# Kernel optimization log

Measured on AMD Instinct MI355X. Metric: run time of the kernel, lower is better.

## Reference

```python
import jax, jax.numpy as jnp
import numpy as np

N_STEPS = 7
N_TERMS = 4


def _sobel_kernel2d():
    dx = jnp.array([[-1.0, 0.0, 1.0], [-2.0, 0.0, 2.0], [-1.0, 0.0, 1.0]], dtype=jnp.float32)
    dy = jnp.array([[-1.0, -2.0, -1.0], [0.0, 0.0, 0.0], [1.0, 2.0, 1.0]], dtype=jnp.float32)
    return 0.125 * jnp.stack([dy, dx, dy, dx], 0)[:, None]  # [4,1,3,3]


def _grid_sample_bilinear(src, sx, sy):
    # src: [N,C,H,W]; sx,sy: [N,H,W] pixel coords (align_corners=False, zeros padding)
    N, C, H, W = src.shape
    x0 = jnp.floor(sx)
    y0 = jnp.floor(sy)
    wx = (sx - x0)[:, None]  # [N,1,H,W]
    wy = (sy - y0)[:, None]
    x0i = x0.astype(jnp.int32)
    y0i = y0.astype(jnp.int32)

    def gather(yi, xi):
        valid = ((xi >= 0) & (xi < W) & (yi >= 0) & (yi < H))
        xc = jnp.clip(xi, 0, W - 1)
        yc = jnp.clip(yi, 0, H - 1)
        v = jax.vmap(lambda im, y, x: im[:, y, x])(src, yc, xc)  # [N,C,H,W]
        return v * valid[:, None].astype(src.dtype)

    v00 = gather(y0i, x0i)
    v01 = gather(y0i, x0i + 1)
    v10 = gather(y0i + 1, x0i)
    v11 = gather(y0i + 1, x0i + 1)
    return (v00 * (1 - wx) * (1 - wy) + v01 * wx * (1 - wy)
            + v10 * (1 - wx) * wy + v11 * wx * wy)


def _transform(src, disp, gy, gx, H, W):
    # new pixel locations; torch normalizes with (size-1) but samples with
    # align_corners=False, net mapping: p -> p*S/(S-1) - 0.5
    py = gy + disp[:, 0]
    px = gx + disp[:, 1]
    sy = py * (H / (H - 1)) - 0.5
    sx = px * (W / (W - 1)) - 0.5
    return _grid_sample_bilinear(src, sx, sy)


def _jacobian2d(vel):
    # replicate-pad then depthwise sobel conv -> [N,2,2,H,W]
    N, _, H, W = vel.shape
    padded = jnp.pad(vel, ((0, 0), (0, 0), (1, 1), (1, 1)), mode='edge')
    jac = jax.lax.conv_general_dilated(
        padded, _sobel_kernel2d(), window_strides=(1, 1), padding='VALID',
        feature_group_count=2, dimension_numbers=('NCHW', 'OIHW', 'NCHW'))
    return jac.reshape(N, 2, 2, H, W)


def _logdet1p(jac, eps):
    # -sum_n (-eps)^n tr(J^n)/n over the 2x2 dims, per pixel -> [N,H,W]
    ld = jnp.zeros(jac.shape[:1] + jac.shape[-2:], dtype=jac.dtype)
    xn = jac
    for n in range(1, N_TERMS + 1):
        if n > 1:
            xn = jnp.einsum('nikhw,nkjhw->nijhw', xn, jac)
        tr = xn[:, 0, 0] + xn[:, 1, 1]
        ld = ld - ((-eps) ** n) * tr / n
    return ld


def _integrate(vel, logdet_jac):
    N, _, H, W = vel.shape
    gy, gx = jnp.meshgrid(jnp.arange(H, dtype=vel.dtype),
                          jnp.arange(W, dtype=vel.dtype), indexing='ij')
    eps = 2.0 ** (-N_STEPS)
    disp = eps * vel
    if logdet_jac:
        ldjac = _logdet1p(_jacobian2d(vel), eps)[:, None]  # [N,1,H,W]
    else:
        ldjac = None
    for _ in range(N_STEPS):
        disp = disp + _transform(disp, disp, gy, gx, H, W)
        if logdet_jac:
            ldjac = ldjac + _transform(ldjac, disp, gy, gx, H, W)
    return disp, ldjac


def setup_inputs() -> dict:
    key = jax.random.key(0)
    vel = jax.random.normal(key, (16, 2, 512, 512), dtype=jnp.float32)
    return {"vel": vel, "logdet_jac": 1}


def reference(vel, logdet_jac):
    return _integrate(vel, bool(logdet_jac))
```

## Files before the change

### kernel.cpp

```cpp
#include <hip/hip_runtime.h>


#define NB 16
#define HH 512
#define WW 512
#define HW (HH * WW)
#define TOT (NB * HW)
#define EPS 0.0078125f
#define DISP_ELEMS (NB * 2 * HW)

typedef _Float16 f16;
typedef _Float16 f16x2 __attribute__((ext_vector_type(2)));

struct Samp {
    int i00, i01, i10, i11;
    float w00, w01, w10, w11;
};

__device__ __forceinline__ Samp make_samp(float sy, float sx) {
    float fy = floorf(sy), fx = floorf(sx);
    float wy = sy - fy, wx = sx - fx;
    int y0 = (int)fy, x0 = (int)fx;
    int y1 = y0 + 1, x1 = x0 + 1;
    bool xv0 = (unsigned)x0 < (unsigned)WW;
    bool xv1 = (unsigned)x1 < (unsigned)WW;
    bool yv0 = (unsigned)y0 < (unsigned)HH;
    bool yv1 = (unsigned)y1 < (unsigned)HH;
    int xc0 = min(max(x0, 0), WW - 1), xc1 = min(max(x1, 0), WW - 1);
    int yc0 = min(max(y0, 0), HH - 1), yc1 = min(max(y1, 0), HH - 1);
    Samp s;
    s.i00 = yc0 * WW + xc0; s.i01 = yc0 * WW + xc1;
    s.i10 = yc1 * WW + xc0; s.i11 = yc1 * WW + xc1;
    float omwx = 1.0f - wx, omwy = 1.0f - wy;
    s.w00 = (xv0 && yv0) ? omwx * omwy : 0.0f;
    s.w01 = (xv1 && yv0) ? wx * omwy   : 0.0f;
    s.w10 = (xv0 && yv1) ? omwx * wy   : 0.0f;
    s.w11 = (xv1 && yv1) ? wx * wy     : 0.0f;
    return s;
}

__global__ void __launch_bounds__(256) init_kernel(const float* __restrict__ vel,
                                                   f16x2* __restrict__ ddst,
                                                   f16* __restrict__ ldst) {
    int idx = blockIdx.x * 256 + threadIdx.x;
    int n = idx >> 18;
    int rem = idx & (HW - 1);
    int y = rem >> 9, x = rem & (WW - 1);

    const float* v0 = vel + (size_t)n * 2 * HW;
    const float* v1 = v0 + HW;

    float c0 = v0[rem], c1 = v1[rem];
    f16x2 dd; dd.x = (f16)(EPS * c0); dd.y = (f16)(EPS * c1);
    ddst[(size_t)n * HW + rem] = dd;

    int ym = max(y - 1, 0), yp = min(y + 1, HH - 1);
    int xm = max(x - 1, 0), xp = min(x + 1, WW - 1);
    int rmm = ym * WW + xm, rm0 = ym * WW + x, rmp = ym * WW + xp;
    int r0m = y * WW + xm,                    r0p = y * WW + xp;
    int rpm = yp * WW + xm, rp0 = yp * WW + x, rpp = yp * WW + xp;

    float a, b, c, d;
    {
        float tmm = v0[rmm], tm0 = v0[rm0], tmp = v0[rmp];
        float t0m = v0[r0m],                t0p = v0[r0p];
        float tpm = v0[rpm], tp0 = v0[rp0], tpp = v0[rpp];
        a = 0.125f * ((tpm + 2.0f * tp0 + tpp) - (tmm + 2.0f * tm0 + tmp));
        b = 0.125f * ((tmp + 2.0f * t0p + tpp) - (tmm + 2.0f * t0m + tpm));
    }
    {
        float tmm = v1[rmm], tm0 = v1[rm0], tmp = v1[rmp];
        float t0m = v1[r0m],                t0p = v1[r0p];
        float tpm = v1[rpm], tp0 = v1[rp0], tpp = v1[rpp];
        c = 0.125f * ((tpm + 2.0f * tp0 + tpp) - (tmm + 2.0f * tm0 + tmp));
        d = 0.125f * ((tmp + 2.0f * t0p + tpp) - (tmm + 2.0f * t0m + tpm));
    }

    float xa = a, xb = b, xc = c, xd = d;
    float ld = EPS * (xa + xd);
    float na = xa * a + xb * c, nb = xa * b + xb * d;
    float nc = xc * a + xd * c, nd = xc * b + xd * d;
    xa = na; xb = nb; xc = nc; xd = nd;
    ld -= (EPS * EPS) * (xa + xd) * 0.5f;
    na = xa * a + xb * c; nb = xa * b + xb * d;
    nc = xc * a + xd * c; nd = xc * b + xd * d;
    xa = na; xb = nb; xc = nc; xd = nd;
    ld += (EPS * EPS * EPS) * (xa + xd) * (1.0f / 3.0f);
    na = xa * a + xb * c;
    nd = xc * b + xd * d;
    ld -= (EPS * EPS * EPS * EPS) * (na + nd) * 0.25f;

    ldst[(size_t)n * HW + rem] = (f16)ld;
}

template <bool FINAL>
__global__ void __launch_bounds__(256) step_kernel(const f16x2* __restrict__ dsrc,
                                                   const f16* __restrict__ lsrc,
                                                   f16x2* __restrict__ ddst,
                                                   f16* __restrict__ ldst,
                                                   float* __restrict__ doutp,
                                                   float* __restrict__ loutp) {
    int bid = blockIdx.x;
    int task = ((bid & 7) << 11) | (bid >> 3);
    int idx = task * 256 + threadIdx.x;
    int n = idx >> 18;
    int rem = idx & (HW - 1);
    int y = rem >> 9, x = rem & (WW - 1);

    const float SC = 512.0f / 511.0f;

    const f16x2* dp = dsrc + (size_t)n * HW;
    f16x2 dv = dp[rem];
    float d0 = (float)dv.x, d1 = (float)dv.y;

    float sy = ((float)y + d0) * SC - 0.5f;
    float sx = ((float)x + d1) * SC - 0.5f;
    Samp s = make_samp(sy, sx);

    f16x2 g00 = dp[s.i00], g01 = dp[s.i01], g10 = dp[s.i10], g11 = dp[s.i11];
    float nd0 = d0 + s.w00 * (float)g00.x + s.w01 * (float)g01.x
                   + s.w10 * (float)g10.x + s.w11 * (float)g11.x;
    float nd1 = d1 + s.w00 * (float)g00.y + s.w01 * (float)g01.y
                   + s.w10 * (float)g10.y + s.w11 * (float)g11.y;

    if (FINAL) {
        float* pd = doutp + (size_t)n * 2 * HW;
        pd[rem] = nd0;
        pd[HW + rem] = nd1;
    } else {
        f16x2 w; w.x = (f16)nd0; w.y = (f16)nd1;
        ddst[(size_t)n * HW + rem] = w;
    }

    float sy2 = ((float)y + nd0) * SC - 0.5f;
    float sx2 = ((float)x + nd1) * SC - 0.5f;
    Samp s2 = make_samp(sy2, sx2);

    const f16* lp = lsrc + (size_t)n * HW;
    float l = (float)lp[rem];
    float nl = l + s2.w00 * (float)lp[s2.i00] + s2.w01 * (float)lp[s2.i01]
                 + s2.w10 * (float)lp[s2.i10] + s2.w11 * (float)lp[s2.i11];
    if (FINAL) {
        loutp[(size_t)n * HW + rem] = nl;
    } else {
        ldst[(size_t)n * HW + rem] = (f16)nl;
    }
}

extern "C" void kernel_launch(void* const* d_in, const int* in_sizes, int n_in,
                              void* d_out, int out_size, void* d_ws, size_t ws_size,
                              hipStream_t stream) {
    const float* vel = (const float*)d_in[0];
    float* out = (float*)d_out;

    f16*   baseA = (f16*)d_out;
    f16*   baseB = (f16*)d_ws;
    f16x2* dA = (f16x2*)baseA;
    f16*   lA = baseA + (size_t)2 * TOT;
    f16x2* dB = (f16x2*)baseB;
    f16*   lB = baseB + (size_t)2 * TOT;

    dim3 grid(TOT / 256), block(256);

    init_kernel<<<grid, block, 0, stream>>>(vel, dB, lB);

    const f16x2* ds = dB;
    const f16*   ls = lB;
    for (int s = 0; s < 6; ++s) {
        f16x2* dd  = (s & 1) ? dB : dA;
        f16*   ldd = (s & 1) ? lB : lA;
        step_kernel<false><<<grid, block, 0, stream>>>(ds, ls, dd, ldd, nullptr, nullptr);
        ds = dd; ls = ldd;
    }
    step_kernel<true><<<grid, block, 0, stream>>>(ds, ls, nullptr, nullptr,
                                                  out, out + DISP_ELEMS);
}
```

Measured before the change: 143.9 us.

## Skew ldjac update one step so both fields share the same bilinear samples

In the reference, each step's ldjac update samples at the freshly updated displacement. That position is the same one the next step's displacement update samples at. The pipeline is restructured into a displacement-only first step, then fused steps that sample disp(k) and ldjac(k-1) with a single set of indices and weights, then a final step that only updates ldjac and writes out. This removes the second make_samp and the dependent second gather round per step, and lets the displacement and ldjac gathers issue together. The cost is an extra kernel launch, and all buffers now live in the workspace, which needs about 48 MB.

```diff
diff --git a/kernel.cpp b/kernel.cpp
--- a/kernel.cpp
+++ b/kernel.cpp
@@ -8,6 +8,7 @@
 #define TOT (NB * HW)
 #define EPS 0.0078125f
 #define DISP_ELEMS (NB * 2 * HW)
+#define SC (512.0f / 511.0f)
 
 typedef _Float16 f16;
 typedef _Float16 f16x2 __attribute__((ext_vector_type(2)));
@@ -93,28 +94,25 @@
     ldst[(size_t)n * HW + rem] = (f16)ld;
 }
 
-template <bool FINAL>
-__global__ void __launch_bounds__(256) step_kernel(const f16x2* __restrict__ dsrc,
-                                                   const f16* __restrict__ lsrc,
-                                                   f16x2* __restrict__ ddst,
-                                                   f16* __restrict__ ldst,
-                                                   float* __restrict__ doutp,
-                                                   float* __restrict__ loutp) {
+__device__ __forceinline__ int remap_idx() {
     int bid = blockIdx.x;
     int task = ((bid & 7) << 11) | (bid >> 3);
-    int idx = task * 256 + threadIdx.x;
-    int n = idx >> 18;
-    int rem = idx & (HW - 1);
-    int y = rem >> 9, x = rem & (WW - 1);
-
-    const float SC = 512.0f / 511.0f;
+    return task * 256 + threadIdx.x;
+}
+
+__global__ void __launch_bounds__(256) step_disp(const f16x2* __restrict__ dsrc,
+                                                 f16x2* __restrict__ ddst) {
+    int idx = remap_idx();
+    int n = idx >> 18;
+    int rem = idx & (HW - 1);
+    int y = rem >> 9, x = rem & (WW - 1);
 
     const f16x2* dp = dsrc + (size_t)n * HW;
     f16x2 dv = dp[rem];
     float d0 = (float)dv.x, d1 = (float)dv.y;
 
-    float sy = ((float)y + d0) * SC - 0.5f;
-    float sx = ((float)x + d1) * SC - 0.5f;
+    float sy = fmaf((float)y + d0, SC, -0.5f);
+    float sx = fmaf((float)x + d1, SC, -0.5f);
     Samp s = make_samp(sy, sx);
 
     f16x2 g00 = dp[s.i00], g01 = dp[s.i01], g10 = dp[s.i10], g11 = dp[s.i11];
@@ -123,28 +121,72 @@
     float nd1 = d1 + s.w00 * (float)g00.y + s.w01 * (float)g01.y
                    + s.w10 * (float)g10.y + s.w11 * (float)g11.y;
 
-    if (FINAL) {
-        float* pd = doutp + (size_t)n * 2 * HW;
-        pd[rem] = nd0;
-        pd[HW + rem] = nd1;
-    } else {
-        f16x2 w; w.x = (f16)nd0; w.y = (f16)nd1;
-        ddst[(size_t)n * HW + rem] = w;
-    }
-
-    float sy2 = ((float)y + nd0) * SC - 0.5f;
-    float sx2 = ((float)x + nd1) * SC - 0.5f;
-    Samp s2 = make_samp(sy2, sx2);
-
-    const f16* lp = lsrc + (size_t)n * HW;
-    float l = (float)lp[rem];
-    float nl = l + s2.w00 * (float)lp[s2.i00] + s2.w01 * (float)lp[s2.i01]
-                 + s2.w10 * (float)lp[s2.i10] + s2.w11 * (float)lp[s2.i11];
-    if (FINAL) {
-        loutp[(size_t)n * HW + rem] = nl;
-    } else {
-        ldst[(size_t)n * HW + rem] = (f16)nl;
-    }
+    f16x2 w; w.x = (f16)nd0; w.y = (f16)nd1;
+    ddst[(size_t)n * HW + rem] = w;
+}
+
+__global__ void __launch_bounds__(256) step_full(const f16x2* __restrict__ dsrc,
+                                                 const f16* __restrict__ lsrc,
+                                                 f16x2* __restrict__ ddst,
+                                                 f16* __restrict__ ldst) {
+    int idx = remap_idx();
+    int n = idx >> 18;
+    int rem = idx & (HW - 1);
+    int y = rem >> 9, x = rem & (WW - 1);
+
+    const f16x2* dp = dsrc + (size_t)n * HW;
+    const f16*   lp = lsrc + (size_t)n * HW;
+
+    f16x2 dv = dp[rem];
+    f16   lv = lp[rem];
+    float d0 = (float)dv.x, d1 = (float)dv.y;
+
+    float sy = fmaf((float)y + d0, SC, -0.5f);
+    float sx = fmaf((float)x + d1, SC, -0.5f);
+    Samp s = make_samp(sy, sx);
+
+    f16x2 g00 = dp[s.i00], g01 = dp[s.i01], g10 = dp[s.i10], g11 = dp[s.i11];
+    f16   h00 = lp[s.i00], h01 = lp[s.i01], h10 = lp[s.i10], h11 = lp[s.i11];
+
+    float nd0 = d0 + s.w00 * (float)g00.x + s.w01 * (float)g01.x
+                   + s.w10 * (float)g10.x + s.w11 * (float)g11.x;
+    float nd1 = d1 + s.w00 * (float)g00.y + s.w01 * (float)g01.y
+                   + s.w10 * (float)g10.y + s.w11 * (float)g11.y;
+    float nl  = (float)lv + s.w00 * (float)h00 + s.w01 * (float)h01
+                          + s.w10 * (float)h10 + s.w11 * (float)h11;
+
+    f16x2 w; w.x = (f16)nd0; w.y = (f16)nd1;
+    ddst[(size_t)n * HW + rem] = w;
+    ldst[(size_t)n * HW + rem] = (f16)nl;
+}
+
+__global__ void __launch_bounds__(256) step_final(const f16x2* __restrict__ dsrc,
+                                                  const f16* __restrict__ lsrc,
+                                                  float* __restrict__ doutp,
+                                                  float* __restrict__ loutp) {
+    int idx = remap_idx();
+    int n = idx >> 18;
+    int rem = idx & (HW - 1);
+    int y = rem >> 9, x = rem & (WW - 1);
+
+    const f16x2* dp = dsrc + (size_t)n * HW;
+    const f16*   lp = lsrc + (size_t)n * HW;
+
+    f16x2 dv = dp[rem];
+    f16   lv = lp[rem];
+    float d0 = (float)dv.x, d1 = (float)dv.y;
+
+    float sy = fmaf((float)y + d0, SC, -0.5f);
+    float sx = fmaf((float)x + d1, SC, -0.5f);
+    Samp s = make_samp(sy, sx);
+
+    float nl = (float)lv + s.w00 * (float)lp[s.i00] + s.w01 * (float)lp[s.i01]
+                         + s.w10 * (float)lp[s.i10] + s.w11 * (float)lp[s.i11];
+
+    float* pd = doutp + (size_t)n * 2 * HW;
+    pd[rem]      = d0;
+    pd[HW + rem] = d1;
+    loutp[(size_t)n * HW + rem] = nl;
 }
 
 extern "C" void kernel_launch(void* const* d_in, const int* in_sizes, int n_in,
@@ -153,25 +195,21 @@
     const float* vel = (const float*)d_in[0];
     float* out = (float*)d_out;
 
-    f16*   baseA = (f16*)d_out;
-    f16*   baseB = (f16*)d_ws;
-    f16x2* dA = (f16x2*)baseA;
-    f16*   lA = baseA + (size_t)2 * TOT;
-    f16x2* dB = (f16x2*)baseB;
-    f16*   lB = baseB + (size_t)2 * TOT;
+    char* wsb = (char*)d_ws;
+    f16x2* dB = (f16x2*)wsb;
+    f16x2* dC = (f16x2*)(wsb + (size_t)16 * 1024 * 1024);
+    f16*   lB = (f16*)  (wsb + (size_t)32 * 1024 * 1024);
+    f16*   lA = (f16*)  (wsb + (size_t)40 * 1024 * 1024);
 
     dim3 grid(TOT / 256), block(256);
 
     init_kernel<<<grid, block, 0, stream>>>(vel, dB, lB);
-
-    const f16x2* ds = dB;
-    const f16*   ls = lB;
-    for (int s = 0; s < 6; ++s) {
-        f16x2* dd  = (s & 1) ? dB : dA;
-        f16*   ldd = (s & 1) ? lB : lA;
-        step_kernel<false><<<grid, block, 0, stream>>>(ds, ls, dd, ldd, nullptr, nullptr);
-        ds = dd; ls = ldd;
-    }
-    step_kernel<true><<<grid, block, 0, stream>>>(ds, ls, nullptr, nullptr,
-                                                  out, out + DISP_ELEMS);
-}
+    step_disp<<<grid, block, 0, stream>>>(dB, dC);
+    step_full<<<grid, block, 0, stream>>>(dC, lB, dB, lA);
+    step_full<<<grid, block, 0, stream>>>(dB, lA, dC, lB);
+    step_full<<<grid, block, 0, stream>>>(dC, lB, dB, lA);
+    step_full<<<grid, block, 0, stream>>>(dB, lA, dC, lB);
+    step_full<<<grid, block, 0, stream>>>(dC, lB, dB, lA);
+    step_full<<<grid, block, 0, stream>>>(dB, lA, dC, lB);
+    step_final<<<grid, block, 0, stream>>>(dC, lB, out, out + DISP_ELEMS);
+}
```

Measured after the change: 137.1 us. -4.7%, faster.
